# Kernel optimization log

Measured on AMD Instinct MI355X. Metric: run time of the kernel, lower is better.

Reference implementation:

```python
import jax, jax.numpy as jnp
import numpy as np

NEG_POS_RATIO = 3

def hard_negative_mining(bg_loss, labels, neg_pos_ratio):
    # bg_loss: [B, P] = -log_softmax(conf)[..., 0]; labels: [B, P] int
    pos_mask = labels > 0                               # [B, P]
    num_pos = jnp.sum(pos_mask, axis=1, keepdims=True)  # [B, 1]
    num_neg = num_pos * neg_pos_ratio                   # [B, 1]
    # positives are excluded from the negative ranking
    masked = jnp.where(pos_mask, -jnp.inf, bg_loss)
    # rank of each prior when sorted by loss descending (0 = hardest negative)
    order = jnp.argsort(jnp.argsort(-masked, axis=1), axis=1)
    neg_mask = order < num_neg
    return pos_mask | neg_mask

def setup_inputs() -> dict:
    key = jax.random.key(0)
    k1, k2, k3, k4, k5 = jax.random.split(key, 5)
    B, P, C = 64, 8732, 81
    pred_loc = jax.random.normal(k1, (B, P, 4), dtype=jnp.float32)
    pred_conf = jax.random.normal(k2, (B, P, C), dtype=jnp.float32)
    gt_loc = jax.random.normal(k3, (B, P, 4), dtype=jnp.float32)
    raw_labels = jax.random.randint(k4, (B, P), 0, C)
    is_pos = jax.random.uniform(k5, (B, P)) < 0.02
    gt_labels = jnp.where(is_pos, raw_labels, 0).astype(jnp.int32)
    return {"pred_loc": pred_loc, "pred_conf": pred_conf, "gt_loc": gt_loc, "gt_labels": gt_labels}

def reference(pred_loc, pred_conf, gt_loc, gt_labels):
    # SSD MultiBox loss (training-mode forward of MultiBoxHeads)
    logp = jax.nn.log_softmax(pred_conf, axis=-1)           # [B, P, C]
    bg_loss = -logp[..., 0]                                 # [B, P]
    mask = jax.lax.stop_gradient(
        hard_negative_mining(jax.lax.stop_gradient(bg_loss), gt_labels, NEG_POS_RATIO))
    # cross-entropy with gt labels, summed over kept (pos + hard-neg) priors
    ce = -jnp.take_along_axis(logp, gt_labels[..., None].astype(jnp.int32), axis=-1)[..., 0]
    objectness_loss = jnp.sum(jnp.where(mask, ce, 0.0))
    # smooth L1 on positive priors only
    pos_mask = gt_labels > 0                                # [B, P]
    diff = pred_loc - gt_loc
    absd = jnp.abs(diff)
    sl1 = jnp.where(absd < 1.0, 0.5 * diff * diff, absd - 0.5)
    smooth_l1_loss = jnp.sum(jnp.where(pos_mask[..., None], sl1, 0.0))
    num_pos = jnp.maximum(jnp.sum(pos_mask), 1).astype(jnp.float32)
    return (objectness_loss / num_pos, smooth_l1_loss / num_pos)
```

## Files before the change

kernel.cpp:

```cpp
#include <hip/hip_runtime.h>
#include <cstdint>
#include <cstddef>

#define BATCH 64
#define PRI   8732
#define NCLS  81
#define NEGPOS 3
#define NTOT  (BATCH * PRI)
#define PPB   64
#define NBLK1 (NTOT / PPB)
#define WFLOATS (PPB * NCLS)
#define WF4   (WFLOATS / 4)

__device__ __forceinline__ unsigned keymap(float f) {
    unsigned u = __float_as_uint(f);
    return (u & 0x80000000u) ? ~u : (u | 0x80000000u);
}

__global__ __launch_bounds__(256) void k_lse(const float* __restrict__ conf,
                                             const int* __restrict__ labels,
                                             const float* __restrict__ ploc,
                                             const float* __restrict__ gloc,
                                             unsigned* __restrict__ keysg,
                                             float* __restrict__ cepart,
                                             float* __restrict__ slpart) {
    __shared__ float lds[WFLOATS + 16];
    __shared__ int   labs[PPB];
    __shared__ float red0[4], red1[4];
    const int t = threadIdx.x;
    const int b = blockIdx.x;

    const float4* g4 = reinterpret_cast<const float4*>(conf) + (size_t)b * WF4;
    float4* l4 = reinterpret_cast<float4*>(lds);
#pragma unroll
    for (int j = 0; j < 5; ++j) l4[t + 256 * j] = g4[t + 256 * j];
    if (t < WF4 - 1280) l4[t + 1280] = g4[t + 1280];
    if (t < PPB) labs[t] = labels[b * PPB + t];
    __syncthreads();

    const int q   = t >> 2, h = t & 3;
    const int f0  = q * NCLS + 20 * h;
    const int len = (h == 3) ? 21 : 20;
    const int a0  = f0 & ~3;
    const int o   = f0 & 3;
    const int ve  = o + len;

    const float4* lp = reinterpret_cast<const float4*>(lds + a0);
    float4 v0 = lp[0], v1 = lp[1], v2 = lp[2], v3 = lp[3], v4 = lp[4], v5 = lp[5];
    v0.x = (o > 0) ? -INFINITY : v0.x;
    v0.y = (o > 1) ? -INFINITY : v0.y;
    v0.z = (o > 2) ? -INFINITY : v0.z;
    v5.x = (ve > 20) ? v5.x : -INFINITY;
    v5.y = (ve > 21) ? v5.y : -INFINITY;
    v5.z = (ve > 22) ? v5.z : -INFINITY;
    v5.w = (ve > 23) ? v5.w : -INFINITY;

    float m;
    {
        float a = fmaxf(fmaxf(v0.x, v0.y), fmaxf(v0.z, v0.w));
        float c = fmaxf(fmaxf(v1.x, v1.y), fmaxf(v1.z, v1.w));
        float d = fmaxf(fmaxf(v2.x, v2.y), fmaxf(v2.z, v2.w));
        float e = fmaxf(fmaxf(v3.x, v3.y), fmaxf(v3.z, v3.w));
        float f = fmaxf(fmaxf(v4.x, v4.y), fmaxf(v4.z, v4.w));
        float g = fmaxf(fmaxf(v5.x, v5.y), fmaxf(v5.z, v5.w));
        m = fmaxf(fmaxf(fmaxf(a, c), fmaxf(d, e)), fmaxf(f, g));
    }
    float s =
        __expf(v0.x - m) + __expf(v0.y - m) + __expf(v0.z - m) + __expf(v0.w - m) +
        __expf(v1.x - m) + __expf(v1.y - m) + __expf(v1.z - m) + __expf(v1.w - m) +
        __expf(v2.x - m) + __expf(v2.y - m) + __expf(v2.z - m) + __expf(v2.w - m) +
        __expf(v3.x - m) + __expf(v3.y - m) + __expf(v3.z - m) + __expf(v3.w - m) +
        __expf(v4.x - m) + __expf(v4.y - m) + __expf(v4.z - m) + __expf(v4.w - m) +
        __expf(v5.x - m) + __expf(v5.y - m) + __expf(v5.z - m) + __expf(v5.w - m);

#pragma unroll
    for (int off = 1; off <= 2; off <<= 1) {
        const float mo = __shfl_xor(m, off, 64);
        const float so = __shfl_xor(s, off, 64);
        const float mn = fmaxf(m, mo);
        s = s * __expf(m - mn) + so * __expf(mo - mn);
        m = mn;
    }
    const float lse = m + __logf(s);

    float cep = 0.0f, sl = 0.0f;
    if (h == 0) {
        const int p   = b * PPB + q;
        const int lab = labs[q];
        const float c0 = lds[q * NCLS];
        unsigned key = 0u;
        if (lab > 0) {
            cep = lse - lds[q * NCLS + lab];
            const float4 pl = *reinterpret_cast<const float4*>(ploc + (size_t)p * 4);
            const float4 gl = *reinterpret_cast<const float4*>(gloc + (size_t)p * 4);
            float d, a;
            d = pl.x - gl.x; a = fabsf(d); sl += (a < 1.0f) ? 0.5f * d * d : a - 0.5f;
            d = pl.y - gl.y; a = fabsf(d); sl += (a < 1.0f) ? 0.5f * d * d : a - 0.5f;
            d = pl.z - gl.z; a = fabsf(d); sl += (a < 1.0f) ? 0.5f * d * d : a - 0.5f;
            d = pl.w - gl.w; a = fabsf(d); sl += (a < 1.0f) ? 0.5f * d * d : a - 0.5f;
        } else {
            key = keymap(lse - c0);
        }
        keysg[p] = key;
    }

#pragma unroll
    for (int off = 32; off > 0; off >>= 1) {
        cep += __shfl_xor(cep, off, 64);
        sl  += __shfl_xor(sl,  off, 64);
    }
    const int wid = t >> 6, lane = t & 63;
    if (lane == 0) { red0[wid] = cep; red1[wid] = sl; }
    __syncthreads();
    if (t == 0) {
        cepart[b] = red0[0] + red0[1] + red0[2] + red0[3];
        slpart[b] = red1[0] + red1[1] + red1[2] + red1[3];
    }
}

__global__ __launch_bounds__(1024) void k_row(const unsigned* __restrict__ keysg,
                                              float* __restrict__ rowobj,
                                              float* __restrict__ rownp) {
    __shared__ unsigned keys_s[PRI];
    __shared__ unsigned hist[16][257];
    __shared__ unsigned ured[16];
    __shared__ float    fred[16];
    __shared__ unsigned sh_prefix, sh_r;
    __shared__ int      sh_flag;

    const int row  = blockIdx.x;
    const int tid  = threadIdx.x;
    const int wid  = tid >> 6;
    const int lane = tid & 63;
    const unsigned* krow = keysg + (size_t)row * PRI;

    unsigned np = 0;
    for (int j = tid; j < PRI; j += 1024) {
        const unsigned key = krow[j];
        keys_s[j] = key;
        np += (key == 0u) ? 1u : 0u;
    }
#pragma unroll
    for (int off = 32; off > 0; off >>= 1) np += __shfl_xor(np, off, 64);
    if (lane == 0) ured[wid] = np;
    __syncthreads();
    unsigned num_pos = 0;
#pragma unroll
    for (int w = 0; w < 16; ++w) num_pos += ured[w];
    const int k = (int)num_pos * NEGPOS;

    unsigned Kstar = 0xFFFFFFFFu;
    int r_eq = 0;
    bool take_all = false;
    if (k > 0) {
        unsigned prefix = 0;
        int r = k, flag = 0;
        unsigned* hist_flat = &hist[0][0];
        for (int level = 3; level >= 0; --level) {
            const int shift = level * 8;
            for (int i = tid; i < 16 * 257; i += 1024) hist_flat[i] = 0;
            __syncthreads();
            for (int j = tid; j < PRI; j += 1024) {
                const unsigned key = keys_s[j];
                if (key == 0u) continue;
                if (level < 3 && (key >> (shift + 8)) != (prefix >> (shift + 8))) continue;
                atomicAdd(&hist[wid][(key >> shift) & 255u], 1u);
            }
            __syncthreads();
            if (wid == 0) {
                const int b0 = lane * 4;
                unsigned h0 = 0, h1 = 0, h2 = 0, h3 = 0;
#pragma unroll
                for (int w = 0; w < 16; ++w) {
                    h0 += hist[w][b0]; h1 += hist[w][b0 + 1];
                    h2 += hist[w][b0 + 2]; h3 += hist[w][b0 + 3];
                }
                const unsigned loc = h0 + h1 + h2 + h3;
                unsigned ssum = loc;
#pragma unroll
                for (int o2 = 1; o2 < 64; o2 <<= 1) {
                    const unsigned t2 = __shfl_down(ssum, o2, 64);
                    if (lane + o2 < 64) ssum += t2;
                }
                const unsigned above = ssum - loc;
                const unsigned cum3 = above + h3;
                const unsigned cum2 = cum3 + h2;
                const unsigned cum1 = cum2 + h1;
                const unsigned cum0 = cum1 + h0;
                const unsigned long long msk = __ballot(cum0 >= (unsigned)r);
                if (msk == 0ULL) {
                    if (lane == 0) sh_flag = 1;
                } else {
                    const int L = 63 - __clzll(msk);
                    if (lane == L) {
                        unsigned selbin, cumsel, hsel;
                        if      (cum3 >= (unsigned)r) { selbin = b0 + 3; cumsel = cum3; hsel = h3; }
                        else if (cum2 >= (unsigned)r) { selbin = b0 + 2; cumsel = cum2; hsel = h2; }
                        else if (cum1 >= (unsigned)r) { selbin = b0 + 1; cumsel = cum1; hsel = h1; }
                        else                          { selbin = b0;     cumsel = cum0; hsel = h0; }
                        sh_prefix = prefix | (selbin << shift);
                        sh_r = (unsigned)r - (cumsel - hsel);
                        sh_flag = 0;
                    }
                }
            }
            __syncthreads();
            flag = sh_flag;
            if (flag) break;
            prefix = sh_prefix;
            r = (int)sh_r;
        }
        take_all = (flag != 0);
        if (!take_all) { Kstar = prefix; r_eq = r; }
    }

    float obj = 0.0f;
    if (k > 0) {
        for (int j = tid; j < PRI; j += 1024) {
            const unsigned key = keys_s[j];
            if (key != 0u && (take_all || key > Kstar))
                obj += __uint_as_float(key ^ 0x80000000u);
        }
        if (tid == 0 && !take_all)
            obj += (float)r_eq * __uint_as_float(Kstar ^ 0x80000000u);
    }

#pragma unroll
    for (int off = 32; off > 0; off >>= 1) obj += __shfl_xor(obj, off, 64);
    __syncthreads();
    if (lane == 0) fred[wid] = obj;
    __syncthreads();
    if (tid == 0) {
        float to = 0.0f;
#pragma unroll
        for (int w = 0; w < 16; ++w) to += fred[w];
        rowobj[row] = to;
        rownp[row]  = (float)num_pos;
    }
}

__global__ __launch_bounds__(256) void k_final(const float* __restrict__ cepart,
                                               const float* __restrict__ slpart,
                                               const float* __restrict__ rowobj,
                                               const float* __restrict__ rownp,
                                               float* __restrict__ out) {
    const int tid = threadIdx.x;
    float ce = 0.0f, sl = 0.0f;
    for (int i = tid; i < NBLK1; i += 256) { ce += cepart[i]; sl += slpart[i]; }
    float ro = 0.0f, np = 0.0f;
    if (tid < BATCH) { ro = rowobj[tid]; np = rownp[tid]; }
#pragma unroll
    for (int off = 32; off > 0; off >>= 1) {
        ce += __shfl_xor(ce, off, 64);
        sl += __shfl_xor(sl, off, 64);
        ro += __shfl_xor(ro, off, 64);
        np += __shfl_xor(np, off, 64);
    }
    __shared__ float r0[4], r1[4], r2[4], r3[4];
    const int wid = tid >> 6, lane = tid & 63;
    if (lane == 0) { r0[wid] = ce; r1[wid] = sl; r2[wid] = ro; r3[wid] = np; }
    __syncthreads();
    if (tid == 0) {
        const float tce = r0[0] + r0[1] + r0[2] + r0[3];
        const float tsl = r1[0] + r1[1] + r1[2] + r1[3];
        const float tro = r2[0] + r2[1] + r2[2] + r2[3];
        const float tnp = r3[0] + r3[1] + r3[2] + r3[3];
        const float npos = fmaxf(tnp, 1.0f);
        out[0] = (tce + tro) / npos;
        out[1] = tsl / npos;
    }
}

extern "C" void kernel_launch(void* const* d_in, const int* in_sizes, int n_in,
                              void* d_out, int out_size, void* d_ws, size_t ws_size,
                              hipStream_t stream) {
    const float* pred_loc  = (const float*)d_in[0];
    const float* pred_conf = (const float*)d_in[1];
    const float* gt_loc    = (const float*)d_in[2];
    const int*   gt_labels = (const int*)d_in[3];
    float* out = (float*)d_out;

    unsigned* keysg   = (unsigned*)d_ws;
    float*    cepart  = (float*)(keysg + NTOT);
    float*    slpart  = cepart + NBLK1;
    float*    rowobj  = slpart + NBLK1;
    float*    rownp   = rowobj + BATCH;

    k_lse<<<NBLK1, 256, 0, stream>>>(pred_conf, gt_labels, pred_loc, gt_loc,
                                     keysg, cepart, slpart);
    k_row<<<BATCH, 1024, 0, stream>>>(keysg, rowobj, rownp);
    k_final<<<1, 256, 0, stream>>>(cepart, slpart, rowobj, rownp, out);
}
```

Measured before the change: 64.79 us.

## Make LSE kernel persistent with double-buffered async global-to-LDS staging

The per-window logsumexp kernel becomes a persistent grid of 768 blocks, each looping over 64-prior windows. The next window's confidence tile is loaded straight into a second LDS buffer with global_load_lds while the current one is reduced. This aims to overlap HBM streaming with compute, cut the launch and tail cost of thousands of short blocks, and shrink the partial-sum arrays the final kernel has to reduce. In exchange it doubles LDS use per block, which can limit how many blocks fit on each CU, and it relies on the barrier to wait for the async LDS writes.

Measured after the change: 57.38 us (median of 2 runs). 1.13x faster.

```diff
diff --git a/kernel.cpp b/kernel.cpp
--- a/kernel.cpp
+++ b/kernel.cpp
@@ -8,13 +8,20 @@
 #define NEGPOS 3
 #define NTOT  (BATCH * PRI)
 #define PPB   64
-#define NBLK1 (NTOT / PPB)
+#define NWIN  (NTOT / PPB)
 #define WFLOATS (PPB * NCLS)
 #define WF4   (WFLOATS / 4)
+#define NPERS 768
 
 __device__ __forceinline__ unsigned keymap(float f) {
     unsigned u = __float_as_uint(f);
     return (u & 0x80000000u) ? ~u : (u | 0x80000000u);
+}
+
+__device__ __forceinline__ void gl_lds16(const float4* g, float4* l) {
+    __builtin_amdgcn_global_load_lds(
+        (const __attribute__((address_space(1))) void*)(const void*)g,
+        (__attribute__((address_space(3))) void*)(void*)l, 16, 0, 0);
 }
 
 __global__ __launch_bounds__(256) void k_lse(const float* __restrict__ conf,
@@ -24,97 +31,116 @@
                                              unsigned* __restrict__ keysg,
                                              float* __restrict__ cepart,
                                              float* __restrict__ slpart) {
-    __shared__ float lds[WFLOATS + 16];
-    __shared__ int   labs[PPB];
+    __shared__ float lds[2][WFLOATS];
+    __shared__ int   labs[2][PPB];
     __shared__ float red0[4], red1[4];
     const int t = threadIdx.x;
-    const int b = blockIdx.x;
-
-    const float4* g4 = reinterpret_cast<const float4*>(conf) + (size_t)b * WF4;
-    float4* l4 = reinterpret_cast<float4*>(lds);
-#pragma unroll
-    for (int j = 0; j < 5; ++j) l4[t + 256 * j] = g4[t + 256 * j];
-    if (t < WF4 - 1280) l4[t + 1280] = g4[t + 1280];
-    if (t < PPB) labs[t] = labels[b * PPB + t];
-    __syncthreads();
-
-    const int q   = t >> 2, h = t & 3;
-    const int f0  = q * NCLS + 20 * h;
-    const int len = (h == 3) ? 21 : 20;
-    const int a0  = f0 & ~3;
-    const int o   = f0 & 3;
-    const int ve  = o + len;
-
-    const float4* lp = reinterpret_cast<const float4*>(lds + a0);
-    float4 v0 = lp[0], v1 = lp[1], v2 = lp[2], v3 = lp[3], v4 = lp[4], v5 = lp[5];
-    v0.x = (o > 0) ? -INFINITY : v0.x;
-    v0.y = (o > 1) ? -INFINITY : v0.y;
-    v0.z = (o > 2) ? -INFINITY : v0.z;
-    v5.x = (ve > 20) ? v5.x : -INFINITY;
-    v5.y = (ve > 21) ? v5.y : -INFINITY;
-    v5.z = (ve > 22) ? v5.z : -INFINITY;
-    v5.w = (ve > 23) ? v5.w : -INFINITY;
-
-    float m;
-    {
-        float a = fmaxf(fmaxf(v0.x, v0.y), fmaxf(v0.z, v0.w));
-        float c = fmaxf(fmaxf(v1.x, v1.y), fmaxf(v1.z, v1.w));
-        float d = fmaxf(fmaxf(v2.x, v2.y), fmaxf(v2.z, v2.w));
-        float e = fmaxf(fmaxf(v3.x, v3.y), fmaxf(v3.z, v3.w));
-        float f = fmaxf(fmaxf(v4.x, v4.y), fmaxf(v4.z, v4.w));
-        float g = fmaxf(fmaxf(v5.x, v5.y), fmaxf(v5.z, v5.w));
-        m = fmaxf(fmaxf(fmaxf(a, c), fmaxf(d, e)), fmaxf(f, g));
-    }
-    float s =
-        __expf(v0.x - m) + __expf(v0.y - m) + __expf(v0.z - m) + __expf(v0.w - m) +
-        __expf(v1.x - m) + __expf(v1.y - m) + __expf(v1.z - m) + __expf(v1.w - m) +
-        __expf(v2.x - m) + __expf(v2.y - m) + __expf(v2.z - m) + __expf(v2.w - m) +
-        __expf(v3.x - m) + __expf(v3.y - m) + __expf(v3.z - m) + __expf(v3.w - m) +
-        __expf(v4.x - m) + __expf(v4.y - m) + __expf(v4.z - m) + __expf(v4.w - m) +
-        __expf(v5.x - m) + __expf(v5.y - m) + __expf(v5.z - m) + __expf(v5.w - m);
-
-#pragma unroll
-    for (int off = 1; off <= 2; off <<= 1) {
-        const float mo = __shfl_xor(m, off, 64);
-        const float so = __shfl_xor(s, off, 64);
-        const float mn = fmaxf(m, mo);
-        s = s * __expf(m - mn) + so * __expf(mo - mn);
-        m = mn;
-    }
-    const float lse = m + __logf(s);
-
-    float cep = 0.0f, sl = 0.0f;
-    if (h == 0) {
-        const int p   = b * PPB + q;
-        const int lab = labs[q];
-        const float c0 = lds[q * NCLS];
-        unsigned key = 0u;
-        if (lab > 0) {
-            cep = lse - lds[q * NCLS + lab];
-            const float4 pl = *reinterpret_cast<const float4*>(ploc + (size_t)p * 4);
-            const float4 gl = *reinterpret_cast<const float4*>(gloc + (size_t)p * 4);
-            float d, a;
-            d = pl.x - gl.x; a = fabsf(d); sl += (a < 1.0f) ? 0.5f * d * d : a - 0.5f;
-            d = pl.y - gl.y; a = fabsf(d); sl += (a < 1.0f) ? 0.5f * d * d : a - 0.5f;
-            d = pl.z - gl.z; a = fabsf(d); sl += (a < 1.0f) ? 0.5f * d * d : a - 0.5f;
-            d = pl.w - gl.w; a = fabsf(d); sl += (a < 1.0f) ? 0.5f * d * d : a - 0.5f;
-        } else {
-            key = keymap(lse - c0);
-        }
-        keysg[p] = key;
+    const int bid = blockIdx.x;
+
+    float ceacc = 0.0f, slacc = 0.0f;
+
+    auto stage = [&](int buf, int w) {
+        const float4* g4 = reinterpret_cast<const float4*>(conf) + (size_t)w * WF4;
+        float4* l4 = reinterpret_cast<float4*>(&lds[buf][0]);
+#pragma unroll
+        for (int j = 0; j < 5; ++j) gl_lds16(&g4[t + 256 * j], &l4[t + 256 * j]);
+        if (t < WF4 - 1280) gl_lds16(&g4[t + 1280], &l4[t + 1280]);
+        if (t < PPB) labs[buf][t] = labels[w * PPB + t];
+    };
+
+    stage(0, bid);
+    __syncthreads();
+
+    int cur = 0;
+    for (int i = 0; ; ++i) {
+        const int w  = bid + i * NPERS;
+        const int wn = w + NPERS;
+        const bool more = (wn < NWIN);
+        if (more) stage(cur ^ 1, wn);
+
+        const float* ldsw = &lds[cur][0];
+        const int q   = t >> 2, h = t & 3;
+        const int f0  = q * NCLS + 20 * h;
+        const int len = (h == 3) ? 21 : 20;
+        const int a0  = f0 & ~3;
+        const int o   = f0 & 3;
+        const int ve  = o + len;
+
+        const float4* lp = reinterpret_cast<const float4*>(ldsw + a0);
+        float4 v0 = lp[0], v1 = lp[1], v2 = lp[2], v3 = lp[3], v4 = lp[4], v5 = lp[5];
+        v0.x = (o > 0) ? -INFINITY : v0.x;
+        v0.y = (o > 1) ? -INFINITY : v0.y;
+        v0.z = (o > 2) ? -INFINITY : v0.z;
+        v5.x = (ve > 20) ? v5.x : -INFINITY;
+        v5.y = (ve > 21) ? v5.y : -INFINITY;
+        v5.z = (ve > 22) ? v5.z : -INFINITY;
+        v5.w = (ve > 23) ? v5.w : -INFINITY;
+
+        float m;
+        {
+            float a = fmaxf(fmaxf(v0.x, v0.y), fmaxf(v0.z, v0.w));
+            float c = fmaxf(fmaxf(v1.x, v1.y), fmaxf(v1.z, v1.w));
+            float d = fmaxf(fmaxf(v2.x, v2.y), fmaxf(v2.z, v2.w));
+            float e = fmaxf(fmaxf(v3.x, v3.y), fmaxf(v3.z, v3.w));
+            float f = fmaxf(fmaxf(v4.x, v4.y), fmaxf(v4.z, v4.w));
+            float g = fmaxf(fmaxf(v5.x, v5.y), fmaxf(v5.z, v5.w));
+            m = fmaxf(fmaxf(fmaxf(a, c), fmaxf(d, e)), fmaxf(f, g));
+        }
+        float s =
+            __expf(v0.x - m) + __expf(v0.y - m) + __expf(v0.z - m) + __expf(v0.w - m) +
+            __expf(v1.x - m) + __expf(v1.y - m) + __expf(v1.z - m) + __expf(v1.w - m) +
+            __expf(v2.x - m) + __expf(v2.y - m) + __expf(v2.z - m) + __expf(v2.w - m) +
+            __expf(v3.x - m) + __expf(v3.y - m) + __expf(v3.z - m) + __expf(v3.w - m) +
+            __expf(v4.x - m) + __expf(v4.y - m) + __expf(v4.z - m) + __expf(v4.w - m) +
+            __expf(v5.x - m) + __expf(v5.y - m) + __expf(v5.z - m) + __expf(v5.w - m);
+
+#pragma unroll
+        for (int off = 1; off <= 2; off <<= 1) {
+            const float mo = __shfl_xor(m, off, 64);
+            const float so = __shfl_xor(s, off, 64);
+            const float mn = fmaxf(m, mo);
+            s = s * __expf(m - mn) + so * __expf(mo - mn);
+            m = mn;
+        }
+        const float lse = m + __logf(s);
+
+        if (h == 0) {
+            const int p   = w * PPB + q;
+            const int lab = labs[cur][q];
+            const float c0 = ldsw[q * NCLS];
+            unsigned key = 0u;
+            if (lab > 0) {
+                ceacc += lse - ldsw[q * NCLS + lab];
+                const float4 pl = *reinterpret_cast<const float4*>(ploc + (size_t)p * 4);
+                const float4 gl = *reinterpret_cast<const float4*>(gloc + (size_t)p * 4);
+                float d, a;
+                d = pl.x - gl.x; a = fabsf(d); slacc += (a < 1.0f) ? 0.5f * d * d : a - 0.5f;
+                d = pl.y - gl.y; a = fabsf(d); slacc += (a < 1.0f) ? 0.5f * d * d : a - 0.5f;
+                d = pl.z - gl.z; a = fabsf(d); slacc += (a < 1.0f) ? 0.5f * d * d : a - 0.5f;
+                d = pl.w - gl.w; a = fabsf(d); slacc += (a < 1.0f) ? 0.5f * d * d : a - 0.5f;
+            } else {
+                key = keymap(lse - c0);
+            }
+            keysg[p] = key;
+        }
+
+        if (!more) break;
+        __syncthreads();
+        cur ^= 1;
     }
 
 #pragma unroll
     for (int off = 32; off > 0; off >>= 1) {
-        cep += __shfl_xor(cep, off, 64);
-        sl  += __shfl_xor(sl,  off, 64);
+        ceacc += __shfl_xor(ceacc, off, 64);
+        slacc += __shfl_xor(slacc, off, 64);
     }
     const int wid = t >> 6, lane = t & 63;
-    if (lane == 0) { red0[wid] = cep; red1[wid] = sl; }
+    __syncthreads();
+    if (lane == 0) { red0[wid] = ceacc; red1[wid] = slacc; }
     __syncthreads();
     if (t == 0) {
-        cepart[b] = red0[0] + red0[1] + red0[2] + red0[3];
-        slpart[b] = red1[0] + red1[1] + red1[2] + red1[3];
+        cepart[bid] = red0[0] + red0[1] + red0[2] + red0[3];
+        slpart[bid] = red1[0] + red1[1] + red1[2] + red1[3];
     }
 }
 
@@ -246,7 +272,7 @@
                                                float* __restrict__ out) {
     const int tid = threadIdx.x;
     float ce = 0.0f, sl = 0.0f;
-    for (int i = tid; i < NBLK1; i += 256) { ce += cepart[i]; sl += slpart[i]; }
+    for (int i = tid; i < NPERS; i += 256) { ce += cepart[i]; sl += slpart[i]; }
     float ro = 0.0f, np = 0.0f;
     if (tid < BATCH) { ro = rowobj[tid]; np = rownp[tid]; }
 #pragma unroll
@@ -282,11 +308,11 @@
 
     unsigned* keysg   = (unsigned*)d_ws;
     float*    cepart  = (float*)(keysg + NTOT);
-    float*    slpart  = cepart + NBLK1;
-    float*    rowobj  = slpart + NBLK1;
+    float*    slpart  = cepart + NPERS;
+    float*    rowobj  = slpart + NPERS;
     float*    rownp   = rowobj + BATCH;
 
-    k_lse<<<NBLK1, 256, 0, stream>>>(pred_conf, gt_labels, pred_loc, gt_loc,
+    k_lse<<<NPERS, 256, 0, stream>>>(pred_conf, gt_labels, pred_loc, gt_loc,
                                      keysg, cepart, slpart);
     k_row<<<BATCH, 1024, 0, stream>>>(keysg, rowobj, rownp);
     k_final<<<1, 256, 0, stream>>>(cepart, slpart, rowobj, rownp, out);
```

## Persistent per-wave triple-buffered LSE kernel with async global-to-LDS loads

Applied to the files above, without the earlier changes.

Turns the logsumexp kernel into a persistent kernel in which each wave processes 16-prior windows. It triple-buffers them in LDS through global_load_lds and manual vmcnt waits, so loads overlap compute and block-wide syncs go away. The positive-prior CE and smooth-L1 work moves into the per-row kernel, which re-reads the labels plus the few needed conf and loc values, and the final reduction gets simpler. The gain depends on whether the hand-written waitcnt values match the real number of outstanding loads; a mismatch could produce races.

Result: faster. 61.91 us (-4.4%).

```diff
diff --git a/kernel.cpp b/kernel.cpp
--- a/kernel.cpp
+++ b/kernel.cpp
@@ -7,124 +7,121 @@
 #define NCLS  81
 #define NEGPOS 3
 #define NTOT  (BATCH * PRI)
-#define PPB   64
-#define NBLK1 (NTOT / PPB)
-#define WFLOATS (PPB * NCLS)
-#define WF4   (WFLOATS / 4)
+#define PW    16
+#define NWINW (NTOT / PW)
+#define WB_F  (PW * NCLS)
+#define WB_F4 (WB_F / 4)
+#define NBLK  512
+#define WAVES_TOT (NBLK * 4)
 
 __device__ __forceinline__ unsigned keymap(float f) {
     unsigned u = __float_as_uint(f);
     return (u & 0x80000000u) ? ~u : (u | 0x80000000u);
 }
 
+__device__ __forceinline__ void gl_lds16(const float4* g, float4* l) {
+    __builtin_amdgcn_global_load_lds(
+        (const __attribute__((address_space(1))) void*)(const void*)g,
+        (__attribute__((address_space(3))) void*)(void*)l, 16, 0, 0);
+}
+
 __global__ __launch_bounds__(256) void k_lse(const float* __restrict__ conf,
-                                             const int* __restrict__ labels,
-                                             const float* __restrict__ ploc,
-                                             const float* __restrict__ gloc,
-                                             unsigned* __restrict__ keysg,
-                                             float* __restrict__ cepart,
-                                             float* __restrict__ slpart) {
-    __shared__ float lds[WFLOATS + 16];
-    __shared__ int   labs[PPB];
-    __shared__ float red0[4], red1[4];
-    const int t = threadIdx.x;
-    const int b = blockIdx.x;
-
-    const float4* g4 = reinterpret_cast<const float4*>(conf) + (size_t)b * WF4;
-    float4* l4 = reinterpret_cast<float4*>(lds);
-#pragma unroll
-    for (int j = 0; j < 5; ++j) l4[t + 256 * j] = g4[t + 256 * j];
-    if (t < WF4 - 1280) l4[t + 1280] = g4[t + 1280];
-    if (t < PPB) labs[t] = labels[b * PPB + t];
-    __syncthreads();
-
-    const int q   = t >> 2, h = t & 3;
-    const int f0  = q * NCLS + 20 * h;
-    const int len = (h == 3) ? 21 : 20;
-    const int a0  = f0 & ~3;
-    const int o   = f0 & 3;
-    const int ve  = o + len;
-
-    const float4* lp = reinterpret_cast<const float4*>(lds + a0);
-    float4 v0 = lp[0], v1 = lp[1], v2 = lp[2], v3 = lp[3], v4 = lp[4], v5 = lp[5];
-    v0.x = (o > 0) ? -INFINITY : v0.x;
-    v0.y = (o > 1) ? -INFINITY : v0.y;
-    v0.z = (o > 2) ? -INFINITY : v0.z;
-    v5.x = (ve > 20) ? v5.x : -INFINITY;
-    v5.y = (ve > 21) ? v5.y : -INFINITY;
-    v5.z = (ve > 22) ? v5.z : -INFINITY;
-    v5.w = (ve > 23) ? v5.w : -INFINITY;
-
-    float m;
-    {
-        float a = fmaxf(fmaxf(v0.x, v0.y), fmaxf(v0.z, v0.w));
-        float c = fmaxf(fmaxf(v1.x, v1.y), fmaxf(v1.z, v1.w));
-        float d = fmaxf(fmaxf(v2.x, v2.y), fmaxf(v2.z, v2.w));
-        float e = fmaxf(fmaxf(v3.x, v3.y), fmaxf(v3.z, v3.w));
-        float f = fmaxf(fmaxf(v4.x, v4.y), fmaxf(v4.z, v4.w));
-        float g = fmaxf(fmaxf(v5.x, v5.y), fmaxf(v5.z, v5.w));
-        m = fmaxf(fmaxf(fmaxf(a, c), fmaxf(d, e)), fmaxf(f, g));
-    }
-    float s =
-        __expf(v0.x - m) + __expf(v0.y - m) + __expf(v0.z - m) + __expf(v0.w - m) +
-        __expf(v1.x - m) + __expf(v1.y - m) + __expf(v1.z - m) + __expf(v1.w - m) +
-        __expf(v2.x - m) + __expf(v2.y - m) + __expf(v2.z - m) + __expf(v2.w - m) +
-        __expf(v3.x - m) + __expf(v3.y - m) + __expf(v3.z - m) + __expf(v3.w - m) +
-        __expf(v4.x - m) + __expf(v4.y - m) + __expf(v4.z - m) + __expf(v4.w - m) +
-        __expf(v5.x - m) + __expf(v5.y - m) + __expf(v5.z - m) + __expf(v5.w - m);
-
-#pragma unroll
-    for (int off = 1; off <= 2; off <<= 1) {
-        const float mo = __shfl_xor(m, off, 64);
-        const float so = __shfl_xor(s, off, 64);
-        const float mn = fmaxf(m, mo);
-        s = s * __expf(m - mn) + so * __expf(mo - mn);
-        m = mn;
-    }
-    const float lse = m + __logf(s);
-
-    float cep = 0.0f, sl = 0.0f;
-    if (h == 0) {
-        const int p   = b * PPB + q;
-        const int lab = labs[q];
-        const float c0 = lds[q * NCLS];
-        unsigned key = 0u;
-        if (lab > 0) {
-            cep = lse - lds[q * NCLS + lab];
-            const float4 pl = *reinterpret_cast<const float4*>(ploc + (size_t)p * 4);
-            const float4 gl = *reinterpret_cast<const float4*>(gloc + (size_t)p * 4);
-            float d, a;
-            d = pl.x - gl.x; a = fabsf(d); sl += (a < 1.0f) ? 0.5f * d * d : a - 0.5f;
-            d = pl.y - gl.y; a = fabsf(d); sl += (a < 1.0f) ? 0.5f * d * d : a - 0.5f;
-            d = pl.z - gl.z; a = fabsf(d); sl += (a < 1.0f) ? 0.5f * d * d : a - 0.5f;
-            d = pl.w - gl.w; a = fabsf(d); sl += (a < 1.0f) ? 0.5f * d * d : a - 0.5f;
-        } else {
-            key = keymap(lse - c0);
-        }
-        keysg[p] = key;
-    }
-
-#pragma unroll
-    for (int off = 32; off > 0; off >>= 1) {
-        cep += __shfl_xor(cep, off, 64);
-        sl  += __shfl_xor(sl,  off, 64);
-    }
-    const int wid = t >> 6, lane = t & 63;
-    if (lane == 0) { red0[wid] = cep; red1[wid] = sl; }
-    __syncthreads();
-    if (t == 0) {
-        cepart[b] = red0[0] + red0[1] + red0[2] + red0[3];
-        slpart[b] = red1[0] + red1[1] + red1[2] + red1[3];
+                                             unsigned* __restrict__ keysg) {
+    __shared__ float lds[4][3][WB_F];
+    const int t = threadIdx.x, wid = t >> 6, lane = t & 63;
+    const int wgl = blockIdx.x * 4 + wid;
+    const float4* conf4 = reinterpret_cast<const float4*>(conf);
+
+    auto stage = [&](int b, int w) {
+        const float4* g4 = conf4 + (size_t)w * WB_F4;
+        float4* l4 = reinterpret_cast<float4*>(&lds[wid][b][0]);
+#pragma unroll
+        for (int j = 0; j < 5; ++j) gl_lds16(&g4[j * 64 + lane], &l4[j * 64 + lane]);
+        if (lane < 4) gl_lds16(&g4[320 + lane], &l4[320 + lane]);
+    };
+
+    stage(0, wgl);
+    stage(1, wgl + WAVES_TOT);
+
+    int b = 0;
+    int w = wgl;
+    for (int i = 0; ; ++i, w += WAVES_TOT) {
+        const int wn1 = w + WAVES_TOT;
+        const int wn2 = w + 2 * WAVES_TOT;
+        if (i == 0)            asm volatile("s_waitcnt vmcnt(6)" ::: "memory");
+        else if (wn1 < NWINW)  asm volatile("s_waitcnt vmcnt(7)" ::: "memory");
+        else                   asm volatile("s_waitcnt vmcnt(1)" ::: "memory");
+        __builtin_amdgcn_sched_barrier(0);
+        if (wn2 < NWINW) stage((b == 0) ? 2 : b - 1, wn2);
+
+        const float* B = &lds[wid][b][0];
+        const int q  = lane >> 2, h = lane & 3;
+        const int f0 = q * NCLS + 20 * h;
+        const int len = (h == 3) ? 21 : 20;
+        const int a0 = f0 & ~3;
+        const int o  = f0 & 3;
+        const int ve = o + len;
+
+        const float4* lp = reinterpret_cast<const float4*>(B + a0);
+        float4 v0 = lp[0], v1 = lp[1], v2 = lp[2], v3 = lp[3], v4 = lp[4], v5 = lp[5];
+        v0.x = (o > 0) ? -INFINITY : v0.x;
+        v0.y = (o > 1) ? -INFINITY : v0.y;
+        v0.z = (o > 2) ? -INFINITY : v0.z;
+        v5.x = (ve > 20) ? v5.x : -INFINITY;
+        v5.y = (ve > 21) ? v5.y : -INFINITY;
+        v5.z = (ve > 22) ? v5.z : -INFINITY;
+        v5.w = (ve > 23) ? v5.w : -INFINITY;
+
+        float m;
+        {
+            float a = fmaxf(fmaxf(v0.x, v0.y), fmaxf(v0.z, v0.w));
+            float c = fmaxf(fmaxf(v1.x, v1.y), fmaxf(v1.z, v1.w));
+            float d = fmaxf(fmaxf(v2.x, v2.y), fmaxf(v2.z, v2.w));
+            float e = fmaxf(fmaxf(v3.x, v3.y), fmaxf(v3.z, v3.w));
+            float f = fmaxf(fmaxf(v4.x, v4.y), fmaxf(v4.z, v4.w));
+            float g = fmaxf(fmaxf(v5.x, v5.y), fmaxf(v5.z, v5.w));
+            m = fmaxf(fmaxf(fmaxf(a, c), fmaxf(d, e)), fmaxf(f, g));
+        }
+        float s =
+            __expf(v0.x - m) + __expf(v0.y - m) + __expf(v0.z - m) + __expf(v0.w - m) +
+            __expf(v1.x - m) + __expf(v1.y - m) + __expf(v1.z - m) + __expf(v1.w - m) +
+            __expf(v2.x - m) + __expf(v2.y - m) + __expf(v2.z - m) + __expf(v2.w - m) +
+            __expf(v3.x - m) + __expf(v3.y - m) + __expf(v3.z - m) + __expf(v3.w - m) +
+            __expf(v4.x - m) + __expf(v4.y - m) + __expf(v4.z - m) + __expf(v4.w - m) +
+            __expf(v5.x - m) + __expf(v5.y - m) + __expf(v5.z - m) + __expf(v5.w - m);
+
+#pragma unroll
+        for (int off = 1; off <= 2; off <<= 1) {
+            const float mo = __shfl_xor(m, off, 64);
+            const float so = __shfl_xor(s, off, 64);
+            const float mn = fmaxf(m, mo);
+            s = s * __expf(m - mn) + so * __expf(mo - mn);
+            m = mn;
+        }
+        const float lse = m + __logf(s);
+
+        if (h == 0) {
+            const float c0 = B[q * NCLS];
+            keysg[(size_t)w * PW + q] = keymap(lse - c0);
+        }
+
+        b = (b == 2) ? 0 : b + 1;
+        if (wn1 >= NWINW) break;
     }
 }
 
 __global__ __launch_bounds__(1024) void k_row(const unsigned* __restrict__ keysg,
+                                              const int* __restrict__ labels,
+                                              const float* __restrict__ conf,
+                                              const float* __restrict__ ploc,
+                                              const float* __restrict__ gloc,
                                               float* __restrict__ rowobj,
+                                              float* __restrict__ rowsl,
                                               float* __restrict__ rownp) {
     __shared__ unsigned keys_s[PRI];
     __shared__ unsigned hist[16][257];
     __shared__ unsigned ured[16];
-    __shared__ float    fred[16];
+    __shared__ float    fred[16], fred2[16];
     __shared__ unsigned sh_prefix, sh_r;
     __shared__ int      sh_flag;
 
@@ -132,13 +129,16 @@
     const int tid  = threadIdx.x;
     const int wid  = tid >> 6;
     const int lane = tid & 63;
-    const unsigned* krow = keysg + (size_t)row * PRI;
+    const unsigned* krow    = keysg  + (size_t)row * PRI;
+    const int*      lab_row = labels + (size_t)row * PRI;
 
     unsigned np = 0;
     for (int j = tid; j < PRI; j += 1024) {
+        const int lab = lab_row[j];
         const unsigned key = krow[j];
-        keys_s[j] = key;
-        np += (key == 0u) ? 1u : 0u;
+        const bool pos = (lab > 0);
+        np += pos ? 1u : 0u;
+        keys_s[j] = pos ? 0u : key;
     }
 #pragma unroll
     for (int off = 32; off > 0; off >>= 1) np += __shfl_xor(np, off, 64);
@@ -225,49 +225,61 @@
             obj += (float)r_eq * __uint_as_float(Kstar ^ 0x80000000u);
     }
 
-#pragma unroll
-    for (int off = 32; off > 0; off >>= 1) obj += __shfl_xor(obj, off, 64);
+    float sl = 0.0f;
+    for (int s2 = 0; s2 < 9; ++s2) {
+        const int j = tid * 9 + s2;
+        if (j >= PRI) break;
+        const int lab = lab_row[j];
+        if (lab > 0) {
+            const size_t p = (size_t)row * PRI + j;
+            const float bg = __uint_as_float(krow[j] ^ 0x80000000u);
+            const float c0 = conf[p * NCLS];
+            const float cl = conf[p * NCLS + (size_t)lab];
+            obj += bg + c0 - cl;
+            const float4 pl = *reinterpret_cast<const float4*>(ploc + p * 4);
+            const float4 gl = *reinterpret_cast<const float4*>(gloc + p * 4);
+            float d, a;
+            d = pl.x - gl.x; a = fabsf(d); sl += (a < 1.0f) ? 0.5f * d * d : a - 0.5f;
+            d = pl.y - gl.y; a = fabsf(d); sl += (a < 1.0f) ? 0.5f * d * d : a - 0.5f;
+            d = pl.z - gl.z; a = fabsf(d); sl += (a < 1.0f) ? 0.5f * d * d : a - 0.5f;
+            d = pl.w - gl.w; a = fabsf(d); sl += (a < 1.0f) ? 0.5f * d * d : a - 0.5f;
+        }
+    }
+
+#pragma unroll
+    for (int off = 32; off > 0; off >>= 1) {
+        obj += __shfl_xor(obj, off, 64);
+        sl  += __shfl_xor(sl,  off, 64);
+    }
     __syncthreads();
-    if (lane == 0) fred[wid] = obj;
+    if (lane == 0) { fred[wid] = obj; fred2[wid] = sl; }
     __syncthreads();
     if (tid == 0) {
-        float to = 0.0f;
-#pragma unroll
-        for (int w = 0; w < 16; ++w) to += fred[w];
+        float to = 0.0f, ts = 0.0f;
+#pragma unroll
+        for (int w = 0; w < 16; ++w) { to += fred[w]; ts += fred2[w]; }
         rowobj[row] = to;
+        rowsl[row]  = ts;
         rownp[row]  = (float)num_pos;
     }
 }
 
-__global__ __launch_bounds__(256) void k_final(const float* __restrict__ cepart,
-                                               const float* __restrict__ slpart,
-                                               const float* __restrict__ rowobj,
-                                               const float* __restrict__ rownp,
-                                               float* __restrict__ out) {
-    const int tid = threadIdx.x;
-    float ce = 0.0f, sl = 0.0f;
-    for (int i = tid; i < NBLK1; i += 256) { ce += cepart[i]; sl += slpart[i]; }
-    float ro = 0.0f, np = 0.0f;
-    if (tid < BATCH) { ro = rowobj[tid]; np = rownp[tid]; }
+__global__ __launch_bounds__(64) void k_final(const float* __restrict__ rowobj,
+                                              const float* __restrict__ rowsl,
+                                              const float* __restrict__ rownp,
+                                              float* __restrict__ out) {
+    const int lane = threadIdx.x;
+    float o = rowobj[lane], s = rowsl[lane], n = rownp[lane];
 #pragma unroll
     for (int off = 32; off > 0; off >>= 1) {
-        ce += __shfl_xor(ce, off, 64);
-        sl += __shfl_xor(sl, off, 64);
-        ro += __shfl_xor(ro, off, 64);
-        np += __shfl_xor(np, off, 64);
-    }
-    __shared__ float r0[4], r1[4], r2[4], r3[4];
-    const int wid = tid >> 6, lane = tid & 63;
-    if (lane == 0) { r0[wid] = ce; r1[wid] = sl; r2[wid] = ro; r3[wid] = np; }
-    __syncthreads();
-    if (tid == 0) {
-        const float tce = r0[0] + r0[1] + r0[2] + r0[3];
-        const float tsl = r1[0] + r1[1] + r1[2] + r1[3];
-        const float tro = r2[0] + r2[1] + r2[2] + r2[3];
-        const float tnp = r3[0] + r3[1] + r3[2] + r3[3];
-        const float npos = fmaxf(tnp, 1.0f);
-        out[0] = (tce + tro) / npos;
-        out[1] = tsl / npos;
+        o += __shfl_xor(o, off, 64);
+        s += __shfl_xor(s, off, 64);
+        n += __shfl_xor(n, off, 64);
+    }
+    if (lane == 0) {
+        const float npos = fmaxf(n, 1.0f);
+        out[0] = o / npos;
+        out[1] = s / npos;
     }
 }
 
@@ -280,14 +292,13 @@
     const int*   gt_labels = (const int*)d_in[3];
     float* out = (float*)d_out;
 
-    unsigned* keysg   = (unsigned*)d_ws;
-    float*    cepart  = (float*)(keysg + NTOT);
-    float*    slpart  = cepart + NBLK1;
-    float*    rowobj  = slpart + NBLK1;
-    float*    rownp   = rowobj + BATCH;
-
-    k_lse<<<NBLK1, 256, 0, stream>>>(pred_conf, gt_labels, pred_loc, gt_loc,
-                                     keysg, cepart, slpart);
-    k_row<<<BATCH, 1024, 0, stream>>>(keysg, rowobj, rownp);
-    k_final<<<1, 256, 0, stream>>>(cepart, slpart, rowobj, rownp, out);
-}
+    unsigned* keysg  = (unsigned*)d_ws;
+    float*    rowobj = (float*)(keysg + NTOT);
+    float*    rowsl  = rowobj + BATCH;
+    float*    rownp  = rowsl + BATCH;
+
+    k_lse<<<NBLK, 256, 0, stream>>>(pred_conf, keysg);
+    k_row<<<BATCH, 1024, 0, stream>>>(keysg, gt_labels, pred_conf,
+                                      pred_loc, gt_loc, rowobj, rowsl, rownp);
+    k_final<<<1, 64, 0, stream>>>(rowobj, rowsl, rownp, out);
+}
```
